# Kernel tuning notes

Hardware: AMD Instinct MI355X
Metric: run time of the kernel (lower is better)

The kernel has to match this reference:

```python
import jax, jax.numpy as jnp
import numpy as np

B, M, HID = 4, 4096, 1024
H, HD = 16, 64          # num_heads, head_dim
SEG = 128               # segment_size
DIL = 2                 # dilation_rate
SCALE = HD ** -0.5


def _hilbert_perm(n_side):
    """Linear indices (y*n+x) visited along a Hilbert curve on an n_side x n_side grid."""
    def d2xy(n, d):
        x = y = 0
        t = d
        s = 1
        while s < n:
            rx = 1 & (t // 2)
            ry = 1 & (t ^ rx)
            if ry == 0:
                if rx == 1:
                    x = s - 1 - x
                    y = s - 1 - y
                x, y = y, x
            x += s * rx
            y += s * ry
            t //= 4
            s *= 2
        return x, y
    idx = np.empty(n_side * n_side, dtype=np.int32)
    for d in range(n_side * n_side):
        x, y = d2xy(n_side, d)
        idx[d] = y * n_side + x
    return idx


def setup_inputs() -> dict:
    key = jax.random.key(0)
    k1, k2, k3 = jax.random.split(key, 3)
    x = jax.random.normal(k1, (B, M, HID), dtype=jnp.float32)
    w_qkv = jax.random.normal(k2, (3 * HID, HID), dtype=jnp.float32) * 0.02
    w_out = jax.random.normal(k3, (HID, HID), dtype=jnp.float32) * 0.02
    hilbert_map = jnp.asarray(_hilbert_perm(int(np.sqrt(M))))  # permutation of [0, M)
    return {"x": x, "w_qkv": w_qkv, "w_out": w_out, "hilbert_map": hilbert_map}


def reference(x, w_qkv, w_out, hilbert_map):
    nseg = M // SEG
    # qkv projection (nn.Linear, no bias): [B, M, 3*HID]
    qkv = x @ w_qkv.T
    qkv = qkv.reshape(B, M, 3, H, HD).transpose(2, 0, 3, 1, 4)  # [3, B, H, M, HD]
    # Hilbert reorder along sequence dim
    qkv = qkv[:, :, :, hilbert_map, :]
    q, k, v = qkv[0], qkv[1], qkv[2]
    # segment into blocks of SEG: [B, H, nseg, SEG, HD]
    q = q.reshape(B, H, nseg, SEG, HD)
    k = k.reshape(B, H, nseg, SEG, HD)
    v = v.reshape(B, H, nseg, SEG, HD)
    scores = jnp.einsum("bhnsd,bhntd->bhnst", q, k) * SCALE
    # dilation mask: position is active if (pos % DIL == 0); pair allowed if row OR col active
    active = (jnp.arange(SEG) % DIL) == 0
    mask = active[:, None] | active[None, :]  # [SEG, SEG]
    scores = jnp.where(mask, scores, jnp.float32(-1e30))
    attn = jax.nn.softmax(scores, axis=-1)
    out = jnp.einsum("bhnst,bhntd->bhnsd", attn, v)  # [B, H, nseg, SEG, HD]
    # output stays in Hilbert order (matches custom autograd semantics)
    out = out.reshape(B, H, M, HD).transpose(0, 2, 1, 3).reshape(B, M, HID)
    return out @ w_out.T
```

## Files before the change

### kernel.cpp

```cpp
#include <hip/hip_runtime.h>
#include <stdint.h>


typedef __attribute__((ext_vector_type(8))) short short8;
typedef __attribute__((ext_vector_type(4))) short short4v;
typedef __attribute__((ext_vector_type(4))) float f32x4;

#define DEV __device__ __forceinline__

DEV short f2bf(float f) {
  union { float f; uint32_t u; } x; x.f = f;
  uint32_t r = x.u + 0x7fffu + ((x.u >> 16) & 1u);
  return (short)(r >> 16);
}

DEV void gload_lds16(const void* g, void* l) {
  __builtin_amdgcn_global_load_lds(
      (const __attribute__((address_space(1))) uint32_t*)g,
      (__attribute__((address_space(3))) uint32_t*)l, 16, 0, 0);
}

#define BAR() __builtin_amdgcn_s_barrier()
#define LGKM0() do { asm volatile("s_waitcnt lgkmcnt(0)" ::: "memory"); \
                     __builtin_amdgcn_sched_barrier(0); } while (0)
#define VMC(n) asm volatile("s_waitcnt vmcnt(" #n ")" ::: "memory")

__global__ __launch_bounds__(256) void k_gather_cast(
    const float* __restrict__ x, const int* __restrict__ perm, short* __restrict__ xp) {
  const int row = blockIdx.x;
  const int b = row >> 12, pos = row & 4095;
  const int src = (b << 12) + perm[pos];
  const f32x4 v = ((const f32x4*)(x + (size_t)src * 1024))[threadIdx.x];
  short4v o = { f2bf(v[0]), f2bf(v[1]), f2bf(v[2]), f2bf(v[3]) };
  ((short4v*)(xp + (size_t)row * 1024))[threadIdx.x] = o;
}

__global__ __launch_bounds__(256) void k_cast(
    const float* __restrict__ src, short* __restrict__ dst) {
  const int i = blockIdx.x * 256 + threadIdx.x;
  const f32x4 v = ((const f32x4*)src)[i];
  short4v o = { f2bf(v[0]), f2bf(v[1]), f2bf(v[2]), f2bf(v[3]) };
  ((short4v*)dst)[i] = o;
}

template <int EPI, int NBJ>
__global__ __launch_bounds__(512, 2) void k_gemm8(
    const short* __restrict__ A, const short* __restrict__ W, void* __restrict__ Cout) {
  __shared__ __attribute__((aligned(16))) short lds[65536];
  const int tid = threadIdx.x;
  const int lane = tid & 63, w = tid >> 6;
  const int wr = w >> 2, wc = w & 3;
  const int lrow = lane & 15, lg = lane >> 4;

  const int nwg = NBJ * 64;
  const int cpx = nwg >> 3;
  const int bid = blockIdx.x;
  const int sw = (bid & 7) * cpx + (bid >> 3);
  const int bi = sw / NBJ, bj = sw % NBJ;

  const short* Abase = A + (size_t)bi * 256 * 1024;
  const short* Bbase = W + (size_t)bj * 256 * 1024;

  const int c0 = tid, c1 = tid + 512;
  const int sOff0 = (c0 >> 3) * 1024 + (((c0 & 7) ^ ((c0 >> 3) & 7)) * 8);
  const int sOff1 = (c1 >> 3) * 1024 + (((c1 & 7) ^ ((c1 >> 3) & 7)) * 8);
  const int pc0 = lg ^ (lrow & 7), pc1 = (4 + lg) ^ (lrow & 7);

  f32x4 acc[2][4][2][2] = {};
  short8 af[4][2], bfrag[2][2][2];

#define ISSUE(base, half, tile, isB) do {                                   \
    const short* _s = (base) + (half) * (128 * 1024) + (tile) * 64;         \
    short* _d = lds + (((tile) & 1) * 32768) + (isB) * 16384 + (half) * 8192; \
    gload_lds16(_s + sOff0, _d + c0 * 8);                                   \
    gload_lds16(_s + sOff1, _d + c1 * 8);                                   \
  } while (0)

#define LDA(mh) do {                                                        \
    const short* _b = ldsbuf + (mh) * 8192;                                 \
    _Pragma("unroll") for (int mi = 0; mi < 4; ++mi) {                      \
      const short* _r = _b + (wr * 64 + mi * 16 + lrow) * 64;               \
      af[mi][0] = *(const short8*)(_r + pc0 * 8);                           \
      af[mi][1] = *(const short8*)(_r + pc1 * 8); } } while (0)

#define LDB(nh) do {                                                        \
    const short* _b = ldsbuf + 16384 + (nh) * 8192;                         \
    _Pragma("unroll") for (int ni = 0; ni < 2; ++ni) {                      \
      const short* _r = _b + (wc * 32 + ni * 16 + lrow) * 64;               \
      bfrag[nh][ni][0] = *(const short8*)(_r + pc0 * 8);                    \
      bfrag[nh][ni][1] = *(const short8*)(_r + pc1 * 8); } } while (0)

#define MM(mh, nh) do {                                                     \
    _Pragma("unroll") for (int mi = 0; mi < 4; ++mi)                        \
    _Pragma("unroll") for (int ni = 0; ni < 2; ++ni) {                      \
      acc[mh][mi][nh][ni] = __builtin_amdgcn_mfma_f32_16x16x32_bf16(        \
          af[mi][0], bfrag[nh][ni][0], acc[mh][mi][nh][ni], 0, 0, 0);       \
      acc[mh][mi][nh][ni] = __builtin_amdgcn_mfma_f32_16x16x32_bf16(        \
          af[mi][1], bfrag[nh][ni][1], acc[mh][mi][nh][ni], 0, 0, 0); } } while (0)

  ISSUE(Abase, 0, 0, 0); ISSUE(Bbase, 0, 0, 1);
  ISSUE(Abase, 1, 0, 0); ISSUE(Bbase, 1, 0, 1);
  ISSUE(Abase, 0, 1, 0); ISSUE(Bbase, 0, 1, 1);
  VMC(4);
  BAR();

#pragma unroll 2
  for (int t = 0; t < 16; ++t) {
    const short* ldsbuf = lds + ((t & 1) * 32768);
    LDA(0); LDB(0);
    if (t + 1 < 16) ISSUE(Abase, 1, t + 1, 0);
    BAR(); LGKM0();
    __builtin_amdgcn_s_setprio(1); MM(0, 0); __builtin_amdgcn_s_setprio(0);
    BAR();
    LDB(1);
    if (t + 1 < 16) ISSUE(Bbase, 1, t + 1, 1);
    BAR(); LGKM0();
    __builtin_amdgcn_s_setprio(1); MM(0, 1); __builtin_amdgcn_s_setprio(0);
    BAR();
    LDA(1);
    if (t + 2 < 16) ISSUE(Abase, 0, t + 2, 0);
    BAR(); LGKM0();
    __builtin_amdgcn_s_setprio(1); MM(1, 0); __builtin_amdgcn_s_setprio(0);
    BAR();
    if (t + 2 < 16) ISSUE(Bbase, 0, t + 2, 1);
    BAR(); LGKM0();
    __builtin_amdgcn_s_setprio(1); MM(1, 1); __builtin_amdgcn_s_setprio(0);
    if (t + 2 < 16) { VMC(4); } else { VMC(0); }
    BAR();
  }
#undef ISSUE
#undef LDA
#undef LDB
#undef MM

  if (EPI == 0) {
    short* Q = (short*)Cout;
#pragma unroll
    for (int mh = 0; mh < 2; ++mh)
#pragma unroll
    for (int mi = 0; mi < 4; ++mi)
#pragma unroll
    for (int reg = 0; reg < 4; ++reg) {
      const int gr = bi * 256 + mh * 128 + wr * 64 + mi * 16 + 4 * lg + reg;
      const int b = gr >> 12, pos = gr & 4095;
#pragma unroll
      for (int nh = 0; nh < 2; ++nh)
#pragma unroll
      for (int ni = 0; ni < 2; ++ni) {
        const int gc = bj * 256 + nh * 128 + wc * 32 + ni * 16 + lrow;
        const int sel = gc >> 10, h = (gc >> 6) & 15, d = gc & 63;
        Q[((((size_t)sel * 4 + b) * 16 + h) * 4096 + pos) * 64 + d] =
            f2bf(acc[mh][mi][nh][ni][reg]);
      }
    }
  } else {
    float* C = (float*)Cout;
#pragma unroll
    for (int mh = 0; mh < 2; ++mh)
#pragma unroll
    for (int mi = 0; mi < 4; ++mi)
#pragma unroll
    for (int reg = 0; reg < 4; ++reg) {
      const int gr = bi * 256 + mh * 128 + wr * 64 + mi * 16 + 4 * lg + reg;
#pragma unroll
      for (int nh = 0; nh < 2; ++nh)
#pragma unroll
      for (int ni = 0; ni < 2; ++ni) {
        const int gc = bj * 256 + nh * 128 + wc * 32 + ni * 16 + lrow;
        C[(size_t)gr * 1024 + gc] = acc[mh][mi][nh][ni][reg];
      }
    }
  }
}

__global__ __launch_bounds__(256, 3) void k_attn(
    const short* __restrict__ qkv, short* __restrict__ aout) {
  __shared__ __attribute__((aligned(16))) short smem[24576];
  short* Qs = smem;
  short* Ks = smem + 8192;
  short* Vt = smem + 16384;
  short* Ps = smem;
  const int bid = blockIdx.x;
  const int seg = bid & 31, h = (bid >> 5) & 15, b = bid >> 9;
  const size_t plane = (size_t)4096 * 64;
  const short* qp = qkv + ((size_t)(0 * 4 + b) * 16 + h) * plane + seg * 128 * 64;
  const short* kp = qkv + ((size_t)(1 * 4 + b) * 16 + h) * plane + seg * 128 * 64;
  const short* vp = qkv + ((size_t)(2 * 4 + b) * 16 + h) * plane + seg * 128 * 64;
  const int tid = threadIdx.x, lane = tid & 63, w = tid >> 6;
  const int lrow = lane & 15, lg = lane >> 4;

#pragma unroll
  for (int i = 0; i < 4; ++i) {
    int c = i * 256 + tid;
    int row = c >> 3, ch = c & 7, g = ch ^ (row & 7);
    gload_lds16(qp + row * 64 + g * 8, &Qs[c * 8]);
    gload_lds16(kp + row * 64 + g * 8, &Ks[c * 8]);
  }
#pragma unroll
  for (int i = 0; i < 4; ++i) {
    int c = i * 256 + tid;
    int t = c >> 3, d0 = (c & 7) * 8;
    short8 v = *(const short8*)(vp + t * 64 + d0);
#pragma unroll
    for (int j = 0; j < 8; ++j) {
      int d = d0 + j;
      Vt[d * 128 + (t ^ ((d & 7) * 8))] = v[j];
    }
  }
  __syncthreads();

  f32x4 s[2][8] = {};
  __builtin_amdgcn_s_setprio(1);
#pragma unroll
  for (int kk = 0; kk < 2; ++kk) {
    short8 qa[2];
#pragma unroll
    for (int mi = 0; mi < 2; ++mi) {
      int r = w * 32 + mi * 16 + lrow;
      int pc = (kk * 4 + lg) ^ (r & 7);
      qa[mi] = *(const short8*)&Qs[r * 64 + pc * 8];
    }
#pragma unroll
    for (int ni = 0; ni < 8; ++ni) {
      int r = ni * 16 + lrow;
      int pc = (kk * 4 + lg) ^ (r & 7);
      short8 kb = *(const short8*)&Ks[r * 64 + pc * 8];
#pragma unroll
      for (int mi = 0; mi < 2; ++mi)
        s[mi][ni] = __builtin_amdgcn_mfma_f32_16x16x32_bf16(qa[mi], kb, s[mi][ni], 0, 0, 0);
    }
  }
  __builtin_amdgcn_s_setprio(0);

  float inv[2][4];
  const int oddcol = lane & 1;
#pragma unroll
  for (int mi = 0; mi < 2; ++mi) {
#pragma unroll
    for (int reg = 0; reg < 4; ++reg) {
      float pm = -3.0e38f;
#pragma unroll
      for (int ni = 0; ni < 8; ++ni) {
        float v = s[mi][ni][reg] * 0.125f;
        if ((reg & 1) && oddcol) v = -1.0e30f;
        s[mi][ni][reg] = v;
        pm = fmaxf(pm, v);
      }
#pragma unroll
      for (int off = 1; off < 16; off <<= 1) pm = fmaxf(pm, __shfl_xor(pm, off));
      float sum = 0.f;
#pragma unroll
      for (int ni = 0; ni < 8; ++ni) {
        float p = __expf(s[mi][ni][reg] - pm);
        s[mi][ni][reg] = p;
        sum += p;
      }
#pragma unroll
      for (int off = 1; off < 16; off <<= 1) sum += __shfl_xor(sum, off);
      inv[mi][reg] = 1.0f / sum;
    }
  }

  __syncthreads();

#pragma unroll
  for (int mi = 0; mi < 2; ++mi)
#pragma unroll
    for (int ni = 0; ni < 8; ++ni)
#pragma unroll
      for (int reg = 0; reg < 4; ++reg) {
        int r = w * 32 + mi * 16 + 4 * lg + reg;
        int col = ni * 16 + lrow;
        Ps[r * 128 + (col ^ ((r & 7) * 8))] = f2bf(s[mi][ni][reg]);
      }

  f32x4 o[2][4] = {};
  __builtin_amdgcn_s_setprio(1);
#pragma unroll
  for (int kt = 0; kt < 4; ++kt) {
    short8 pa[2];
#pragma unroll
    for (int mi = 0; mi < 2; ++mi) {
      int r = w * 32 + mi * 16 + lrow;
      int pc = (kt * 4 + lg) ^ (r & 7);
      pa[mi] = *(const short8*)&Ps[r * 128 + pc * 8];
    }
#pragma unroll
    for (int dn = 0; dn < 4; ++dn) {
      int d = dn * 16 + lrow;
      int pc = (kt * 4 + lg) ^ (d & 7);
      short8 vb = *(const short8*)&Vt[d * 128 + pc * 8];
#pragma unroll
      for (int mi = 0; mi < 2; ++mi)
        o[mi][dn] = __builtin_amdgcn_mfma_f32_16x16x32_bf16(pa[mi], vb, o[mi][dn], 0, 0, 0);
    }
  }
  __builtin_amdgcn_s_setprio(0);

#pragma unroll
  for (int mi = 0; mi < 2; ++mi)
#pragma unroll
    for (int dn = 0; dn < 4; ++dn)
#pragma unroll
      for (int reg = 0; reg < 4; ++reg) {
        int r = w * 32 + mi * 16 + 4 * lg + reg;
        int pos = seg * 128 + r;
        int d = dn * 16 + lrow;
        aout[((size_t)(b * 4096 + pos)) * 1024 + h * 64 + d] =
            f2bf(o[mi][dn][reg] * inv[mi][reg]);
      }
}

extern "C" void kernel_launch(void* const* d_in, const int* in_sizes, int n_in,
                              void* d_out, int out_size, void* d_ws, size_t ws_size,
                              hipStream_t stream) {
  const float* x     = (const float*)d_in[0];
  const float* w_qkv = (const float*)d_in[1];
  const float* w_out = (const float*)d_in[2];
  const int*   perm  = (const int*)d_in[3];

  char* ws = (char*)d_ws;
  short* xp   = (short*)(ws);
  short* wq   = (short*)(ws + 33554432);
  short* wo   = (short*)(ws + 33554432 + 6291456);
  short* qkvb = (short*)(ws + 41943040);
  short* aout = xp;

  k_gather_cast<<<16384, 256, 0, stream>>>(x, perm, xp);
  k_cast<<<3072, 256, 0, stream>>>(w_qkv, wq);
  k_cast<<<1024, 256, 0, stream>>>(w_out, wo);
  k_gemm8<0, 12><<<768, 512, 0, stream>>>(xp, wq, qkvb);
  k_attn<<<2048, 256, 0, stream>>>(qkvb, aout);
  k_gemm8<1, 4><<<256, 512, 0, stream>>>(aout, wo, d_out);
}
```

Baseline: 308.9 us.

## Transpose MFMA operand order for vectorized epilogue stores and deepen GEMM prefetch

Swaps the A/B operands of the MFMA calls in the GEMM and attention kernels so that each lane holds four consecutive output columns. This lets the epilogues write packed short4/float4 vectors instead of scattered scalar stores. The softmax is reorganised to match the transposed layout, cutting the row reductions to two cross-lane shuffles, and P is written to LDS as short4. The GEMM prefetch schedule is also shifted one stage earlier, with deeper vmcnt waits and one barrier pair removed. The gains rely on these wider stores and better overlap, with some added risk around LDS/barrier correctness from the changed schedule.

```diff
diff --git a/kernel.cpp b/kernel.cpp
--- a/kernel.cpp
+++ b/kernel.cpp
@@ -12,6 +12,11 @@
   union { float f; uint32_t u; } x; x.f = f;
   uint32_t r = x.u + 0x7fffu + ((x.u >> 16) & 1u);
   return (short)(r >> 16);
+}
+
+DEV short4v pack4(f32x4 v) {
+  short4v o = { f2bf(v[0]), f2bf(v[1]), f2bf(v[2]), f2bf(v[3]) };
+  return o;
 }
 
 DEV void gload_lds16(const void* g, void* l) {
@@ -31,16 +36,14 @@
   const int b = row >> 12, pos = row & 4095;
   const int src = (b << 12) + perm[pos];
   const f32x4 v = ((const f32x4*)(x + (size_t)src * 1024))[threadIdx.x];
-  short4v o = { f2bf(v[0]), f2bf(v[1]), f2bf(v[2]), f2bf(v[3]) };
-  ((short4v*)(xp + (size_t)row * 1024))[threadIdx.x] = o;
+  ((short4v*)(xp + (size_t)row * 1024))[threadIdx.x] = pack4(v);
 }
 
 __global__ __launch_bounds__(256) void k_cast(
     const float* __restrict__ src, short* __restrict__ dst) {
   const int i = blockIdx.x * 256 + threadIdx.x;
   const f32x4 v = ((const f32x4*)src)[i];
-  short4v o = { f2bf(v[0]), f2bf(v[1]), f2bf(v[2]), f2bf(v[3]) };
-  ((short4v*)dst)[i] = o;
+  ((short4v*)dst)[i] = pack4(v);
 }
 
 template <int EPI, int NBJ>
@@ -66,7 +69,7 @@
   const int sOff1 = (c1 >> 3) * 1024 + (((c1 & 7) ^ ((c1 >> 3) & 7)) * 8);
   const int pc0 = lg ^ (lrow & 7), pc1 = (4 + lg) ^ (lrow & 7);
 
-  f32x4 acc[2][4][2][2] = {};
+  f32x4 acc[2][2][2][4] = {};
   short8 af[4][2], bfrag[2][2][2];
 
 #define ISSUE(base, half, tile, isB) do {                                   \
@@ -91,41 +94,41 @@
       bfrag[nh][ni][1] = *(const short8*)(_r + pc1 * 8); } } while (0)
 
 #define MM(mh, nh) do {                                                     \
-    _Pragma("unroll") for (int mi = 0; mi < 4; ++mi)                        \
-    _Pragma("unroll") for (int ni = 0; ni < 2; ++ni) {                      \
-      acc[mh][mi][nh][ni] = __builtin_amdgcn_mfma_f32_16x16x32_bf16(        \
-          af[mi][0], bfrag[nh][ni][0], acc[mh][mi][nh][ni], 0, 0, 0);       \
-      acc[mh][mi][nh][ni] = __builtin_amdgcn_mfma_f32_16x16x32_bf16(        \
-          af[mi][1], bfrag[nh][ni][1], acc[mh][mi][nh][ni], 0, 0, 0); } } while (0)
+    _Pragma("unroll") for (int ni = 0; ni < 2; ++ni)                        \
+    _Pragma("unroll") for (int mi = 0; mi < 4; ++mi) {                      \
+      acc[nh][ni][mh][mi] = __builtin_amdgcn_mfma_f32_16x16x32_bf16(        \
+          bfrag[nh][ni][0], af[mi][0], acc[nh][ni][mh][mi], 0, 0, 0);       \
+      acc[nh][ni][mh][mi] = __builtin_amdgcn_mfma_f32_16x16x32_bf16(        \
+          bfrag[nh][ni][1], af[mi][1], acc[nh][ni][mh][mi], 0, 0, 0); } } while (0)
 
   ISSUE(Abase, 0, 0, 0); ISSUE(Bbase, 0, 0, 1);
   ISSUE(Abase, 1, 0, 0); ISSUE(Bbase, 1, 0, 1);
   ISSUE(Abase, 0, 1, 0); ISSUE(Bbase, 0, 1, 1);
-  VMC(4);
+  ISSUE(Abase, 1, 1, 0);
+  VMC(6);
   BAR();
 
 #pragma unroll 2
   for (int t = 0; t < 16; ++t) {
     const short* ldsbuf = lds + ((t & 1) * 32768);
     LDA(0); LDB(0);
-    if (t + 1 < 16) ISSUE(Abase, 1, t + 1, 0);
+    if (t < 15) ISSUE(Bbase, 1, t + 1, 1);
     BAR(); LGKM0();
     __builtin_amdgcn_s_setprio(1); MM(0, 0); __builtin_amdgcn_s_setprio(0);
     BAR();
     LDB(1);
-    if (t + 1 < 16) ISSUE(Bbase, 1, t + 1, 1);
+    if (t < 14) ISSUE(Abase, 0, t + 2, 0);
     BAR(); LGKM0();
     __builtin_amdgcn_s_setprio(1); MM(0, 1); __builtin_amdgcn_s_setprio(0);
     BAR();
     LDA(1);
-    if (t + 2 < 16) ISSUE(Abase, 0, t + 2, 0);
+    if (t < 14) ISSUE(Bbase, 0, t + 2, 1);
     BAR(); LGKM0();
     __builtin_amdgcn_s_setprio(1); MM(1, 0); __builtin_amdgcn_s_setprio(0);
     BAR();
-    if (t + 2 < 16) ISSUE(Bbase, 0, t + 2, 1);
-    BAR(); LGKM0();
+    if (t < 14) ISSUE(Abase, 1, t + 2, 0);
     __builtin_amdgcn_s_setprio(1); MM(1, 1); __builtin_amdgcn_s_setprio(0);
-    if (t + 2 < 16) { VMC(4); } else { VMC(0); }
+    if (t < 14) { VMC(6); } else { VMC(0); }
     BAR();
   }
 #undef ISSUE
@@ -135,39 +138,37 @@
 
   if (EPI == 0) {
     short* Q = (short*)Cout;
-#pragma unroll
-    for (int mh = 0; mh < 2; ++mh)
-#pragma unroll
-    for (int mi = 0; mi < 4; ++mi)
-#pragma unroll
-    for (int reg = 0; reg < 4; ++reg) {
-      const int gr = bi * 256 + mh * 128 + wr * 64 + mi * 16 + 4 * lg + reg;
-      const int b = gr >> 12, pos = gr & 4095;
-#pragma unroll
-      for (int nh = 0; nh < 2; ++nh)
-#pragma unroll
-      for (int ni = 0; ni < 2; ++ni) {
-        const int gc = bj * 256 + nh * 128 + wc * 32 + ni * 16 + lrow;
-        const int sel = gc >> 10, h = (gc >> 6) & 15, d = gc & 63;
-        Q[((((size_t)sel * 4 + b) * 16 + h) * 4096 + pos) * 64 + d] =
-            f2bf(acc[mh][mi][nh][ni][reg]);
+    const int bb = bi >> 4;
+    const int posc = (bi & 15) * 256 + wr * 64 + lrow;
+#pragma unroll
+    for (int nh = 0; nh < 2; ++nh)
+#pragma unroll
+    for (int ni = 0; ni < 2; ++ni) {
+      const int gc0 = bj * 256 + nh * 128 + wc * 32 + ni * 16;
+      const int sel = gc0 >> 10, h = (gc0 >> 6) & 15;
+      const int dbase = (gc0 & 63) + 4 * lg;
+      short* basep = Q + (((size_t)(sel * 4 + bb) * 16 + h) << 18) + dbase;
+#pragma unroll
+      for (int mh = 0; mh < 2; ++mh)
+#pragma unroll
+      for (int mi = 0; mi < 4; ++mi) {
+        const int pos = posc + mh * 128 + mi * 16;
+        *(short4v*)(basep + (size_t)pos * 64) = pack4(acc[nh][ni][mh][mi]);
       }
     }
   } else {
     float* C = (float*)Cout;
 #pragma unroll
-    for (int mh = 0; mh < 2; ++mh)
-#pragma unroll
-    for (int mi = 0; mi < 4; ++mi)
-#pragma unroll
-    for (int reg = 0; reg < 4; ++reg) {
-      const int gr = bi * 256 + mh * 128 + wr * 64 + mi * 16 + 4 * lg + reg;
-#pragma unroll
-      for (int nh = 0; nh < 2; ++nh)
-#pragma unroll
-      for (int ni = 0; ni < 2; ++ni) {
-        const int gc = bj * 256 + nh * 128 + wc * 32 + ni * 16 + lrow;
-        C[(size_t)gr * 1024 + gc] = acc[mh][mi][nh][ni][reg];
+    for (int nh = 0; nh < 2; ++nh)
+#pragma unroll
+    for (int ni = 0; ni < 2; ++ni) {
+      const int gcb = bj * 256 + nh * 128 + wc * 32 + ni * 16 + 4 * lg;
+#pragma unroll
+      for (int mh = 0; mh < 2; ++mh)
+#pragma unroll
+      for (int mi = 0; mi < 4; ++mi) {
+        const int gr = bi * 256 + mh * 128 + wr * 64 + mi * 16 + lrow;
+        *(f32x4*)(C + (size_t)gr * 1024 + gcb) = acc[nh][ni][mh][mi];
       }
     }
   }
@@ -209,72 +210,73 @@
   }
   __syncthreads();
 
-  f32x4 s[2][8] = {};
+  f32x4 st[8][2] = {};
   __builtin_amdgcn_s_setprio(1);
 #pragma unroll
   for (int kk = 0; kk < 2; ++kk) {
-    short8 qa[2];
-#pragma unroll
-    for (int mi = 0; mi < 2; ++mi) {
-      int r = w * 32 + mi * 16 + lrow;
+    short8 qb[2];
+#pragma unroll
+    for (int nb = 0; nb < 2; ++nb) {
+      int r = w * 32 + nb * 16 + lrow;
       int pc = (kk * 4 + lg) ^ (r & 7);
-      qa[mi] = *(const short8*)&Qs[r * 64 + pc * 8];
-    }
-#pragma unroll
-    for (int ni = 0; ni < 8; ++ni) {
-      int r = ni * 16 + lrow;
+      qb[nb] = *(const short8*)&Qs[r * 64 + pc * 8];
+    }
+#pragma unroll
+    for (int na = 0; na < 8; ++na) {
+      int r = na * 16 + lrow;
       int pc = (kk * 4 + lg) ^ (r & 7);
-      short8 kb = *(const short8*)&Ks[r * 64 + pc * 8];
-#pragma unroll
-      for (int mi = 0; mi < 2; ++mi)
-        s[mi][ni] = __builtin_amdgcn_mfma_f32_16x16x32_bf16(qa[mi], kb, s[mi][ni], 0, 0, 0);
+      short8 ka = *(const short8*)&Ks[r * 64 + pc * 8];
+#pragma unroll
+      for (int nb = 0; nb < 2; ++nb)
+        st[na][nb] = __builtin_amdgcn_mfma_f32_16x16x32_bf16(ka, qb[nb], st[na][nb], 0, 0, 0);
     }
   }
   __builtin_amdgcn_s_setprio(0);
 
-  float inv[2][4];
-  const int oddcol = lane & 1;
-#pragma unroll
-  for (int mi = 0; mi < 2; ++mi) {
-#pragma unroll
-    for (int reg = 0; reg < 4; ++reg) {
-      float pm = -3.0e38f;
-#pragma unroll
-      for (int ni = 0; ni < 8; ++ni) {
-        float v = s[mi][ni][reg] * 0.125f;
-        if ((reg & 1) && oddcol) v = -1.0e30f;
-        s[mi][ni][reg] = v;
+  float inv_sm[2];
+  const int oddS = lrow & 1;
+#pragma unroll
+  for (int nb = 0; nb < 2; ++nb) {
+    float pm = -3.0e38f;
+#pragma unroll
+    for (int na = 0; na < 8; ++na)
+#pragma unroll
+      for (int reg = 0; reg < 4; ++reg) {
+        float v = st[na][nb][reg] * 0.125f;
+        if (oddS && (reg & 1)) v = -1.0e30f;
+        st[na][nb][reg] = v;
         pm = fmaxf(pm, v);
       }
-#pragma unroll
-      for (int off = 1; off < 16; off <<= 1) pm = fmaxf(pm, __shfl_xor(pm, off));
-      float sum = 0.f;
-#pragma unroll
-      for (int ni = 0; ni < 8; ++ni) {
-        float p = __expf(s[mi][ni][reg] - pm);
-        s[mi][ni][reg] = p;
+    pm = fmaxf(pm, __shfl_xor(pm, 16));
+    pm = fmaxf(pm, __shfl_xor(pm, 32));
+    float sum = 0.f;
+#pragma unroll
+    for (int na = 0; na < 8; ++na)
+#pragma unroll
+      for (int reg = 0; reg < 4; ++reg) {
+        float p = __expf(st[na][nb][reg] - pm);
+        st[na][nb][reg] = p;
         sum += p;
       }
-#pragma unroll
-      for (int off = 1; off < 16; off <<= 1) sum += __shfl_xor(sum, off);
-      inv[mi][reg] = 1.0f / sum;
-    }
+    sum += __shfl_xor(sum, 16);
+    sum += __shfl_xor(sum, 32);
+    inv_sm[nb] = 1.0f / sum;
   }
 
   __syncthreads();
 
 #pragma unroll
-  for (int mi = 0; mi < 2; ++mi)
-#pragma unroll
-    for (int ni = 0; ni < 8; ++ni)
-#pragma unroll
-      for (int reg = 0; reg < 4; ++reg) {
-        int r = w * 32 + mi * 16 + 4 * lg + reg;
-        int col = ni * 16 + lrow;
-        Ps[r * 128 + (col ^ ((r & 7) * 8))] = f2bf(s[mi][ni][reg]);
-      }
-
-  f32x4 o[2][4] = {};
+  for (int na = 0; na < 8; ++na)
+#pragma unroll
+    for (int nb = 0; nb < 2; ++nb) {
+      const int s = w * 32 + nb * 16 + lrow;
+      const int t0 = na * 16 + 4 * lg;
+      *(short4v*)&Ps[s * 128 + (((t0 >> 3) ^ (s & 7)) * 8) + (t0 & 7)] =
+          pack4(st[na][nb]);
+    }
+  __syncthreads();
+
+  f32x4 ot[4][2] = {};
   __builtin_amdgcn_s_setprio(1);
 #pragma unroll
   for (int kt = 0; kt < 4; ++kt) {
@@ -292,23 +294,22 @@
       short8 vb = *(const short8*)&Vt[d * 128 + pc * 8];
 #pragma unroll
       for (int mi = 0; mi < 2; ++mi)
-        o[mi][dn] = __builtin_amdgcn_mfma_f32_16x16x32_bf16(pa[mi], vb, o[mi][dn], 0, 0, 0);
+        ot[dn][mi] = __builtin_amdgcn_mfma_f32_16x16x32_bf16(vb, pa[mi], ot[dn][mi], 0, 0, 0);
     }
   }
   __builtin_amdgcn_s_setprio(0);
 
 #pragma unroll
-  for (int mi = 0; mi < 2; ++mi)
-#pragma unroll
-    for (int dn = 0; dn < 4; ++dn)
-#pragma unroll
-      for (int reg = 0; reg < 4; ++reg) {
-        int r = w * 32 + mi * 16 + 4 * lg + reg;
-        int pos = seg * 128 + r;
-        int d = dn * 16 + lrow;
-        aout[((size_t)(b * 4096 + pos)) * 1024 + h * 64 + d] =
-            f2bf(o[mi][dn][reg] * inv[mi][reg]);
-      }
+  for (int dn = 0; dn < 4; ++dn)
+#pragma unroll
+    for (int mi = 0; mi < 2; ++mi) {
+      const int d0 = dn * 16 + 4 * lg;
+      const int pos = seg * 128 + w * 32 + mi * 16 + lrow;
+      const float iv = inv_sm[mi];
+      f32x4 v = ot[dn][mi];
+      f32x4 vs = { v[0] * iv, v[1] * iv, v[2] * iv, v[3] * iv };
+      *(short4v*)&aout[(size_t)(b * 4096 + pos) * 1024 + h * 64 + d0] = pack4(vs);
+    }
 }
 
 extern "C" void kernel_launch(void* const* d_in, const int* in_sizes, int n_in,
```

After: 315.4 us. +2.1%, slower.
